# Kernel tuning notes

Measured on AMD Instinct MI355X. Metric: run time of the kernel, lower is better.

Reference implementation:

```python
import jax, jax.numpy as jnp
import numpy as np

DIM = 1024
NUM_HEAVY = 1024
N_ITERS = 50
EPS = 1.0
FETCH_K_RATIO = 9.0 / 8.0


def rms_norm(x, gamma):
    # F.normalize(x, dim=-1) * sqrt(d) * gamma
    norm = jnp.maximum(jnp.linalg.norm(x, axis=-1, keepdims=True), 1e-12)
    return (x / norm) * (x.shape[-1] ** 0.5) * gamma


def feed_forward(x, gamma, w1, b1, w2, b2):
    h = jax.nn.gelu(rms_norm(x, gamma) @ w1 + b1, approximate=False)
    return h @ w2 + b2


def coor_descent(s, k, n_iters, eps):
    # Wright et al. coordinate descent routing scores (eps_decay=1 -> constant eps)
    logk = jnp.log(jnp.asarray(k, dtype=s.dtype))

    def step(ab, _):
        a, b = ab
        sb = (s + b) / eps
        a = eps * (logk - jax.scipy.special.logsumexp(sb, axis=-1, keepdims=True))
        b = -jax.nn.relu(s + a)
        return (a, b), None

    a0 = jnp.zeros_like(s[..., :1])
    b0 = -s
    (a, b), _ = jax.lax.scan(step, (a0, b0), None, length=n_iters)
    return jnp.exp((s + a + b) / eps)


def setup_inputs() -> dict:
    key = jax.random.key(0)
    ks = jax.random.split(key, 8)
    b, n, d = 4, 8192, DIM
    dl, dh = int(d * 0.5), d * 4
    u = lambda k, shape, fan_in: jax.random.uniform(k, shape, jnp.float32, -1.0, 1.0) / np.sqrt(fan_in)
    return {
        "x": jax.random.normal(ks[0], (b, n, d), jnp.float32),
        "routing_token": jax.random.normal(ks[1], (d,), jnp.float32),
        "light_gamma": jnp.ones((d,), jnp.float32),
        "light_w1": u(ks[2], (d, dl), d),
        "light_b1": jnp.zeros((dl,), jnp.float32),
        "light_w2": u(ks[3], (dl, d), dl),
        "light_b2": jnp.zeros((d,), jnp.float32),
        "heavy_gamma": jnp.ones((d,), jnp.float32),
        "heavy_w1": u(ks[4], (d, dh), d),
        "heavy_b1": jnp.zeros((dh,), jnp.float32),
        "heavy_w2": u(ks[5], (dh, d), dh),
        "heavy_b2": jnp.zeros((d,), jnp.float32),
    }


def reference(x, routing_token, light_gamma, light_w1, light_b1, light_w2, light_b2,
              heavy_gamma, heavy_w1, heavy_b1, heavy_w2, heavy_b2):
    b, n, d = x.shape
    # light branch over all tokens
    light_out = feed_forward(x, light_gamma, light_w1, light_b1, light_w2, light_b2)

    # coordinate-descent router (single routing token)
    s = jnp.einsum('bnd,d->bn', x, routing_token)
    effective_k = min(NUM_HEAVY * FETCH_K_RATIO, n)
    scores = coor_descent(s, effective_k, N_ITERS, EPS)
    sel_scores, sel_idx = jax.lax.top_k(scores, NUM_HEAVY)  # [b, k]
    # straight-through: forward value 1.0, gradient flows through sel_scores
    sel_scores = sel_scores + jax.lax.stop_gradient(1.0 - sel_scores)

    # gather -> heavy FFN -> scale -> scatter back
    routed = jnp.take_along_axis(x, sel_idx[..., None], axis=1)  # [b, k, d]
    routed_out = feed_forward(routed, heavy_gamma, heavy_w1, heavy_b1, heavy_w2, heavy_b2)
    routed_out = routed_out * sel_scores[..., None]
    batch_idx = jnp.arange(b)[:, None]
    heavy_out = jnp.zeros_like(x).at[batch_idx, sel_idx].set(routed_out)

    return light_out + heavy_out
```

## Files before the change

kernel.cpp:

```cpp
#include <hip/hip_runtime.h>
#include <hip/hip_bf16.h>
#include <math.h>

#define DIMD   1024
#define NBATCH 4
#define NSEQ   8192
#define NTOK   (NBATCH * NSEQ)
#define NHEAVY 1024
#define NSEL   (NBATCH * NHEAVY)
#define DLIGHT 512
#define DHEAVY 4096
#define NITERS 50
#define BK     64

typedef __attribute__((ext_vector_type(8))) short short8;
typedef __attribute__((ext_vector_type(4))) float f32x4;
typedef __attribute__((ext_vector_type(4))) unsigned short u16x4;

__device__ __forceinline__ unsigned short f2bf(float f) {
    __hip_bfloat16 h = __float2bfloat16(f);
    union { __hip_bfloat16 h; unsigned short u; } cvt;
    cvt.h = h;
    return cvt.u;
}

__device__ __forceinline__ float bf2f(unsigned short u) {
    return __uint_as_float((unsigned)u << 16);
}

__device__ __forceinline__ float gelu_fast(float x) {
    float ax = fabsf(x) * 0.7071067811865475f;
    float t = 1.0f / fmaf(0.3275911f, ax, 1.0f);
    float p = fmaf(t, 1.061405429f, -1.453152027f);
    p = fmaf(t, p, 1.421413741f);
    p = fmaf(t, p, -0.284496736f);
    p = fmaf(t, p, 0.254829592f);
    p = p * t;
    float e = __expf(-ax * ax);
    float erf_abs = fmaf(-p, e, 1.0f);
    float erf = copysignf(erf_abs, x);
    return 0.5f * x * (1.0f + erf);
}

__device__ __forceinline__ void gload_lds16(const void* g, void* l) {
    __builtin_amdgcn_global_load_lds(
        (const __attribute__((address_space(1))) void*)g,
        (__attribute__((address_space(3))) void*)l,
        16, 0, 0);
}

__global__ __launch_bounds__(256) void fused_init(
    const float* __restrict__ lw1, const float* __restrict__ lw2,
    const float* __restrict__ hw1, const float* __restrict__ hw2,
    const float* __restrict__ lgamma, const float* __restrict__ hgamma,
    short* __restrict__ wl1t, short* __restrict__ wl2t,
    short* __restrict__ wh1t, short* __restrict__ wh2t,
    const float* __restrict__ x, const float* __restrict__ rt,
    unsigned short* __restrict__ xb, float* __restrict__ sc,
    double* __restrict__ s_out, int* __restrict__ inv) {
    __shared__ float tile[32][33];
    __shared__ float red[4];
    __shared__ double redd[4];
    int b = blockIdx.x;
    int tid = threadIdx.x;

    const float* cin = nullptr; short* cout = nullptr; const float* cg = nullptr;
    int cK = 0, cN = 0, cnx = 0, cb = 0;
    if (b < 512)        { cin = lw1; cout = wl1t; cg = lgamma; cK = DIMD;   cN = DLIGHT; cnx = 16;  cb = b; }
    else if (b < 1024)  { cin = lw2; cout = wl2t; cg = nullptr; cK = DLIGHT; cN = DIMD;  cnx = 32;  cb = b - 512; }
    else if (b < 5120)  { cin = hw1; cout = wh1t; cg = hgamma; cK = DIMD;   cN = DHEAVY; cnx = 128; cb = b - 1024; }
    else if (b < 9216)  { cin = hw2; cout = wh2t; cg = nullptr; cK = DHEAVY; cN = DIMD;  cnx = 32;  cb = b - 5120; }

    if (cin) {
        int n0 = (cb % cnx) * 32, k0 = (cb / cnx) * 32;
        int tx = tid & 31, ty = tid >> 5;
        #pragma unroll
        for (int j = 0; j < 4; j++) {
            int k = k0 + ty + 8 * j;
            float g = cg ? cg[k] : 1.0f;
            tile[ty + 8 * j][tx] = cin[(size_t)k * cN + (n0 + tx)] * g;
        }
        __syncthreads();
        #pragma unroll
        for (int j = 0; j < 4; j++)
            cout[(size_t)(n0 + ty + 8 * j) * cK + (k0 + tx)] =
                (short)f2bf(tile[tx][ty + 8 * j]);
        return;
    }

    int t = b - 9216;
    const float4* xr = (const float4*)(x + (size_t)t * DIMD);
    float4 v = xr[tid];
    ushort4 pk;
    pk.x = f2bf(v.x); pk.y = f2bf(v.y); pk.z = f2bf(v.z); pk.w = f2bf(v.w);
    ((ushort4*)(xb + (size_t)t * DIMD))[tid] = pk;

    float ss = v.x * v.x + v.y * v.y + v.z * v.z + v.w * v.w;
    float4 rv = ((const float4*)rt)[tid];
    double sd = (double)v.x * rv.x + (double)v.y * rv.y + (double)v.z * rv.z + (double)v.w * rv.w;
    #pragma unroll
    for (int off = 32; off > 0; off >>= 1) {
        ss += __shfl_down(ss, off);
        sd += __shfl_down(sd, off);
    }
    if ((tid & 63) == 0) { red[tid >> 6] = ss; redd[tid >> 6] = sd; }
    __syncthreads();
    if (tid == 0) {
        s_out[t] = redd[0] + redd[1] + redd[2] + redd[3];
        float tot = red[0] + red[1] + red[2] + red[3];
        sc[t] = 32.0f / fmaxf(sqrtf(tot), 1e-12f);
        inv[t] = -1;
    }
}

__global__ __launch_bounds__(256) void mega_kern(
    const double* __restrict__ s, int* __restrict__ sel, int* __restrict__ inv,
    const short* __restrict__ A, const short* __restrict__ Bt,
    const float* __restrict__ bias, const float* __restrict__ sc,
    __hip_bfloat16* __restrict__ outb) {
    __shared__ alignas(16) char smem[65536 + 64];
    short (*As)[128 * 64] = reinterpret_cast<short (*)[128 * 64]>(smem);
    short (*Bs)[128 * 64] = reinterpret_cast<short (*)[128 * 64]>(smem + 32768);
    int tid = threadIdx.x;

    if (blockIdx.x < 4) {
        int r = blockIdx.x;
        int lw = tid & 63, w = tid >> 6;
        double* redd = (double*)(smem + 65536);
        const double* sr = s + (size_t)r * NSEQ;
        double es[32];
        #pragma unroll
        for (int i = 0; i < 32; i++) es[i] = exp(sr[tid + i * 256]);
        const double Kk = 1152.0;
        double ea = exp(log(Kk) - log((double)NSEQ));
        for (int it = 1; it < NITERS; it++) {
            double loc = 0.0;
            #pragma unroll
            for (int i = 0; i < 32; i++) {
                double p = es[i] * ea;
                loc += (p < 1.0 ? p : 1.0);
            }
            #pragma unroll
            for (int off = 32; off > 0; off >>= 1) loc += __shfl_down(loc, off);
            int pb = (it & 1) * 4;
            if (lw == 0) redd[pb + w] = loc;
            __syncthreads();
            double S = redd[pb] + redd[pb + 1] + redd[pb + 2] + redd[pb + 3];
            ea = ea * (Kk / S);
        }
        double a = log(ea);
        __syncthreads();
        if (tid >= 64) return;

        int l = tid;
        double* sw = (double*)smem;
        int cnt = 0;
        for (int base = 0; base < NSEQ; base += 64) {
            int idx = base + l;
            double v = sr[idx];
            bool sat = (v + a) >= 0.0;
            sw[idx] = sat ? -1.0e300 : v;
            unsigned long long m = __ballot(sat);
            int pre = __popcll(m & ((1ull << l) - 1ull));
            if (sat) {
                int slot = cnt + pre;
                if (slot < NHEAVY) {
                    sel[r * NHEAVY + slot] = r * NSEQ + idx;
                    inv[r * NSEQ + idx] = r * NHEAVY + slot;
                }
            }
            cnt += (int)__popcll(m);
        }
        for (int slot = cnt; slot < NHEAVY; slot++) {
            double best = -1.0e301; int bidx = NSEQ;
            for (int i = 0; i < NSEQ / 64; i++) {
                int idx = i * 64 + l;
                double v = sw[idx];
                if (v > best) { best = v; bidx = idx; }
            }
            #pragma unroll
            for (int off = 32; off > 0; off >>= 1) {
                double ov = __shfl_down(best, off);
                int oi = __shfl_down(bidx, off);
                if (ov > best || (ov == best && oi < bidx)) { best = ov; bidx = oi; }
            }
            bidx = __shfl(bidx, 0);
            if (l == 0) {
                sel[r * NHEAVY + slot] = r * NSEQ + bidx;
                inv[r * NSEQ + bidx] = r * NHEAVY + slot;
                sw[bidx] = -1.0e300;
            }
        }
        return;
    }

    const int N = DLIGHT, K = DIMD;
    int gid = blockIdx.x - 4;
    int id = (gid & 7) * (1024 >> 3) + (gid >> 3);
    int nx = N / 128;
    int bxi = id % nx, byi = id / nx;
    int l = tid & 63, w = tid >> 6;
    int wr = w >> 1, wc = w & 1;
    int bn0 = bxi * 128, bm0 = byi * 128;

    f32x4 zero = {0.f, 0.f, 0.f, 0.f};
    f32x4 acc[4][4];
    #pragma unroll
    for (int i = 0; i < 4; i++)
        #pragma unroll
        for (int j = 0; j < 4; j++) acc[i][j] = zero;

    const short* AgC[4];
    const short* BgC[4];
    #pragma unroll
    for (int c = 0; c < 4; c++) {
        int p = c * 4096 + tid * 16;
        int o = p ^ (((p >> 7) & 7) << 4);
        int lrow = o >> 7, colb = o & 127;
        AgC[c] = A + (size_t)(bm0 + lrow) * K + (colb >> 1);
        BgC[c] = Bt + (size_t)(bn0 + lrow) * K + (colb >> 1);
    }
    const int sbase = (tid & ~63) * 8;

    auto stage = [&](int b, int k0) {
        #pragma unroll
        for (int c = 0; c < 4; c++) {
            gload_lds16(AgC[c] + k0, &As[b][sbase + c * 2048]);
            gload_lds16(BgC[c] + k0, &Bs[b][sbase + c * 2048]);
        }
    };

    const int lr16 = l & 15;
    const int swzm = (lr16 & 7) << 4;
    const int colkm[2] = { ((l >> 4) * 16) ^ swzm, (((l >> 4) * 16) + 64) ^ swzm };

    int nt = K / 64;
    stage(0, 0);
    for (int t = 0; t < nt; ++t) {
        int cur = t & 1;
        if (t + 1 < nt) {
            stage(cur ^ 1, (t + 1) * 64);
            asm volatile("s_waitcnt vmcnt(8)" ::: "memory");
        } else {
            asm volatile("s_waitcnt vmcnt(0)" ::: "memory");
        }
        __builtin_amdgcn_s_barrier();
        asm volatile("" ::: "memory");
        const char* aBuf = (const char*)&As[cur][0];
        const char* bBuf = (const char*)&Bs[cur][0];
        #pragma unroll
        for (int kk = 0; kk < 2; kk++) {
            short8 af[4], bf[4];
            #pragma unroll
            for (int i = 0; i < 4; i++) {
                af[i] = *reinterpret_cast<const short8*>(aBuf + (wr * 64 + i * 16 + lr16) * 128 + colkm[kk]);
                bf[i] = *reinterpret_cast<const short8*>(bBuf + (wc * 64 + i * 16 + lr16) * 128 + colkm[kk]);
            }
            #pragma unroll
            for (int mi = 0; mi < 4; mi++)
                #pragma unroll
                for (int ni = 0; ni < 4; ni++)
                    acc[mi][ni] = __builtin_amdgcn_mfma_f32_16x16x32_bf16(bf[ni], af[mi], acc[mi][ni], 0, 0, 0);
        }
        if (t + 1 < nt) {
            asm volatile("" ::: "memory");
            __builtin_amdgcn_s_barrier();
            asm volatile("" ::: "memory");
        }
    }

    int orow0 = bm0 + wr * 64, ocol0 = bn0 + wc * 64;
    const int lq = (l >> 4) * 4;
    #pragma unroll
    for (int mi = 0; mi < 4; mi++) {
        int row = orow0 + mi * 16 + lr16;
        float scv = sc[row];
        #pragma unroll
        for (int ni = 0; ni < 4; ni++) {
            int c0 = ocol0 + ni * 16 + lq;
            f32x4 bv = *reinterpret_cast<const f32x4*>(bias + c0);
            u16x4 pk;
            #pragma unroll
            for (int rg = 0; rg < 4; rg++)
                pk[rg] = f2bf(gelu_fast(fmaf(scv, acc[mi][ni][rg], bv[rg])));
            *reinterpret_cast<u16x4*>((unsigned short*)outb + (size_t)row * N + c0) = pk;
        }
    }
}

__global__ __launch_bounds__(256) void reduce_hv_kern(
    const unsigned short* __restrict__ phb, const float* __restrict__ hb2,
    float* __restrict__ hv, int nsk) {
    int h = blockIdx.x;
    int c0 = threadIdx.x * 4;
    f32x4 acc = *reinterpret_cast<const f32x4*>(hb2 + c0);
    for (int j = 0; j < nsk; j++) {
        u16x4 p = *reinterpret_cast<const u16x4*>(phb + ((size_t)j * NSEL + h) * DIMD + c0);
        #pragma unroll
        for (int rg = 0; rg < 4; rg++) acc[rg] += bf2f(p[rg]);
    }
    *reinterpret_cast<f32x4*>(hv + (size_t)h * DIMD + c0) = acc;
}

template <int EPI, bool GATHER>
__global__ __launch_bounds__(512) void gemm256(
    const short* __restrict__ A, const short* __restrict__ Bt,
    const float* __restrict__ bias,
    const float* __restrict__ sc, const int* __restrict__ sel,
    const int* __restrict__ inv, const float* __restrict__ hv,
    float* __restrict__ outf, __hip_bfloat16* __restrict__ outb,
    int M, int N, int K) {
    __shared__ alignas(16) short As[2][2][128 * 64];
    __shared__ alignas(16) short Bs[2][2][128 * 64];

    int nx = gridDim.x, ny = gridDim.y;
    int nwg = nx * ny * gridDim.z;
    int id = ((int)blockIdx.z * ny + blockIdx.y) * nx + blockIdx.x;
    if ((nwg & 7) == 0) id = (id & 7) * (nwg >> 3) + (id >> 3);
    int bxi = id % nx; int rem = id / nx;
    int byi = rem % ny; int bz = rem / ny;
    int klen = K / (int)gridDim.z, k0base = bz * klen;
    int bn0 = bxi * 256, bm0 = byi * 256;

    int tid = threadIdx.x;
    int l = tid & 63, w = tid >> 6;
    int wr = w >> 2, wc = w & 3;

    f32x4 zero = {0.f, 0.f, 0.f, 0.f};
    f32x4 acc[8][4];
    #pragma unroll
    for (int i = 0; i < 8; i++)
        #pragma unroll
        for (int j = 0; j < 4; j++) acc[i][j] = zero;

    const short* aSrc[2][2];
    const short* bSrc[2][2];
    #pragma unroll
    for (int h = 0; h < 2; h++)
        #pragma unroll
        for (int j = 0; j < 2; j++) {
            int p = j * 8192 + tid * 16;
            int o = p ^ (((p >> 7) & 7) << 4);
            int lrow = o >> 7, colb = o & 127;
            int agrow = bm0 + h * 128 + lrow;
            int garow = GATHER ? sel[agrow] : agrow;
            aSrc[h][j] = A + (size_t)garow * K + (colb >> 1);
            bSrc[h][j] = Bt + (size_t)(bn0 + h * 128 + lrow) * K + (colb >> 1);
        }

    auto stageA = [&](int b, int h, int kof) {
        #pragma unroll
        for (int j = 0; j < 2; j++)
            gload_lds16(aSrc[h][j] + kof, &As[b][h][j * 4096 + w * 512]);
    };
    auto stageB = [&](int b, int h, int kof) {
        #pragma unroll
        for (int j = 0; j < 2; j++)
            gload_lds16(bSrc[h][j] + kof, &Bs[b][h][j * 4096 + w * 512]);
    };

    int nt = klen / BK;
    stageA(0, 0, k0base); stageA(0, 1, k0base);
    stageB(0, 0, k0base); stageB(0, 1, k0base);
    if (nt > 1) {
        stageB(1, 0, k0base + BK); stageB(1, 1, k0base + BK);
        asm volatile("s_waitcnt vmcnt(4)" ::: "memory");
    } else {
        asm volatile("s_waitcnt vmcnt(0)" ::: "memory");
    }
    __builtin_amdgcn_s_barrier();

    const int lr = l & 15;
    const int swz = (lr & 7) << 4;
    const int rbase = lr * 128;
    const int colk[2] = { (((l >> 4) * 16)) ^ swz, (((l >> 4) * 16) + 64) ^ swz };

    short8 bfr[4][2];
    for (int t = 0; t < nt; ++t) {
        int d = t & 1;
        const char* aHalf = (const char*)(&As[d][wr][0]);
        const char* bHalf = (const char*)(&Bs[d][wc >> 1][0]) + (wc & 1) * 8192;
        #pragma unroll
        for (int ph = 0; ph < 2; ph++) {
            if (ph == 0) {
                #pragma unroll
                for (int ni = 0; ni < 4; ni++)
                    #pragma unroll
                    for (int kk = 0; kk < 2; kk++)
                        bfr[ni][kk] = *reinterpret_cast<const short8*>(bHalf + rbase + ni * 2048 + colk[kk]);
            }
            short8 afr[4][2];
            #pragma unroll
            for (int m2 = 0; m2 < 4; m2++)
                #pragma unroll
                for (int kk = 0; kk < 2; kk++)
                    afr[m2][kk] = *reinterpret_cast<const short8*>(aHalf + rbase + (ph * 4 + m2) * 2048 + colk[kk]);
            if (ph == 0) {
                if (t + 1 < nt) {
                    stageA(d ^ 1, 0, k0base + (t + 1) * BK);
                    stageA(d ^ 1, 1, k0base + (t + 1) * BK);
                }
            } else {
                if (t + 2 < nt) {
                    stageB(d, 0, k0base + (t + 2) * BK);
                    stageB(d, 1, k0base + (t + 2) * BK);
                    asm volatile("s_waitcnt vmcnt(4)" ::: "memory");
                } else {
                    asm volatile("s_waitcnt vmcnt(0)" ::: "memory");
                }
            }
            __builtin_amdgcn_s_barrier();
            asm volatile("s_waitcnt lgkmcnt(0)" ::: "memory");
            __builtin_amdgcn_s_setprio(1);
            #pragma unroll
            for (int m2 = 0; m2 < 4; m2++)
                #pragma unroll
                for (int ni = 0; ni < 4; ni++)
                    #pragma unroll
                    for (int kk = 0; kk < 2; kk++)
                        acc[ph * 4 + m2][ni] = __builtin_amdgcn_mfma_f32_16x16x32_bf16(
                            bfr[ni][kk], afr[m2][kk], acc[ph * 4 + m2][ni], 0, 0, 0);
            __builtin_amdgcn_s_setprio(0);
            __builtin_amdgcn_s_barrier();
        }
    }

    int orow0 = bm0 + wr * 128, ocol0 = bn0 + wc * 64;
    const int lq = (l >> 4) * 4;
    #pragma unroll
    for (int mi = 0; mi < 8; mi++) {
        int row = orow0 + mi * 16 + lr;
        float scv = 0.0f;
        int iv = -1;
        if (EPI == 0) scv = sc[GATHER ? sel[row] : row];
        if (EPI == 3) iv = inv[row];
        #pragma unroll
        for (int ni = 0; ni < 4; ni++) {
            int c0 = ocol0 + ni * 16 + lq;
            if (EPI == 0) {
                f32x4 bv = *reinterpret_cast<const f32x4*>(bias + c0);
                u16x4 pk;
                #pragma unroll
                for (int rg = 0; rg < 4; rg++)
                    pk[rg] = f2bf(gelu_fast(fmaf(scv, acc[mi][ni][rg], bv[rg])));
                *reinterpret_cast<u16x4*>((unsigned short*)outb + (size_t)row * N + c0) = pk;
            } else if (EPI == 2) {
                u16x4 pk;
                #pragma unroll
                for (int rg = 0; rg < 4; rg++) pk[rg] = f2bf(acc[mi][ni][rg]);
                *reinterpret_cast<u16x4*>((unsigned short*)outb + ((size_t)bz * M + row) * (size_t)N + c0) = pk;
            } else {
                f32x4 bv = *reinterpret_cast<const f32x4*>(bias + c0);
                f32x4 v = acc[mi][ni] + bv;
                if (iv >= 0) {
                    f32x4 hvv = *reinterpret_cast<const f32x4*>(hv + (size_t)iv * DIMD + c0);
                    v = v + hvv;
                }
                __builtin_nontemporal_store(v, reinterpret_cast<f32x4*>(outf + (size_t)row * N + c0));
            }
        }
    }
}

extern "C" void kernel_launch(void* const* d_in, const int* in_sizes, int n_in,
                              void* d_out, int out_size, void* d_ws, size_t ws_size,
                              hipStream_t stream) {
    (void)in_sizes; (void)n_in; (void)out_size;
    const float* x      = (const float*)d_in[0];
    const float* rt     = (const float*)d_in[1];
    const float* lgamma = (const float*)d_in[2];
    const float* lw1    = (const float*)d_in[3];
    const float* lb1    = (const float*)d_in[4];
    const float* lw2    = (const float*)d_in[5];
    const float* lb2    = (const float*)d_in[6];
    const float* hgamma = (const float*)d_in[7];
    const float* hw1    = (const float*)d_in[8];
    const float* hb1    = (const float*)d_in[9];
    const float* hw2    = (const float*)d_in[10];
    const float* hb2    = (const float*)d_in[11];
    float* out = (float*)d_out;

    auto rnd = [](size_t b) { return (b + 255) & ~(size_t)255; };
    size_t fixed = rnd(NTOK * sizeof(double))
                 + rnd(NSEL * sizeof(int))
                 + rnd(NTOK * sizeof(int))
                 + rnd(NTOK * sizeof(float))
                 + rnd((size_t)DLIGHT * DIMD * 2)
                 + rnd((size_t)DIMD * DLIGHT * 2)
                 + rnd((size_t)DHEAVY * DIMD * 2)
                 + rnd((size_t)DIMD * DHEAVY * 2)
                 + rnd((size_t)NTOK * DIMD * 2)
                 + rnd((size_t)NSEL * DHEAVY * 2)
                 + rnd((size_t)NTOK * DLIGHT * 2)
                 + rnd((size_t)NSEL * DIMD * 4);
    int nsk = 4;
    while (nsk > 1 && fixed + rnd((size_t)nsk * NSEL * DIMD * 2) > ws_size) nsk >>= 1;

    char* base = (char*)d_ws;
    size_t off = 0;
    auto alloc = [&](size_t bytes) -> void* {
        void* p = base + off;
        off += rnd(bytes);
        return p;
    };
    double* s     = (double*)alloc(NTOK * sizeof(double));
    int*    sel   = (int*)alloc(NSEL * sizeof(int));
    int*    inv   = (int*)alloc(NTOK * sizeof(int));
    float*  sc    = (float*)alloc(NTOK * sizeof(float));
    short*  wl1t  = (short*)alloc((size_t)DLIGHT * DIMD * 2);
    short*  wl2t  = (short*)alloc((size_t)DIMD * DLIGHT * 2);
    short*  wh1t  = (short*)alloc((size_t)DHEAVY * DIMD * 2);
    short*  wh2t  = (short*)alloc((size_t)DIMD * DHEAVY * 2);
    short*  xb    = (short*)alloc((size_t)NTOK * DIMD * 2);
    short*  hh    = (short*)alloc((size_t)NSEL * DHEAVY * 2);
    short*  hl    = (short*)alloc((size_t)NTOK * DLIGHT * 2);
    float*  hv    = (float*)alloc((size_t)NSEL * DIMD * 4);
    short*  phb   = (short*)alloc((size_t)nsk * NSEL * DIMD * 2);

    fused_init<<<9216 + NTOK, 256, 0, stream>>>(
        lw1, lw2, hw1, hw2, lgamma, hgamma,
        wl1t, wl2t, wh1t, wh2t,
        x, rt, (unsigned short*)xb, sc, s, inv);

    mega_kern<<<4 + 1024, 256, 0, stream>>>(
        s, sel, inv, xb, wl1t, lb1, sc, (__hip_bfloat16*)hl);

    gemm256<0, true><<<dim3(DHEAVY / 256, NSEL / 256), 512, 0, stream>>>(
        xb, wh1t, hb1, sc, sel, nullptr, nullptr,
        nullptr, (__hip_bfloat16*)hh, NSEL, DHEAVY, DIMD);
    gemm256<2, false><<<dim3(DIMD / 256, NSEL / 256, nsk), 512, 0, stream>>>(
        hh, wh2t, nullptr, nullptr, nullptr, nullptr, nullptr,
        nullptr, (__hip_bfloat16*)phb, NSEL, DIMD, DHEAVY);
    reduce_hv_kern<<<NSEL, 256, 0, stream>>>((const unsigned short*)phb, hb2, hv, nsk);

    gemm256<3, false><<<dim3(DIMD / 256, NTOK / 256), 512, 0, stream>>>(
        hl, wl2t, lb2, nullptr, nullptr, inv, hv,
        out, nullptr, NTOK, DIMD, DLIGHT);
}
```

Measured before the change: 290.8 us.

## Simplify GEMM pipelines to single-barrier double buffering with full prefetch

Both GEMM kernels move to a plain double-buffered loop. Each iteration issues all global->LDS loads for the next tile up front, computes the current tile, then waits with vmcnt(0) and takes one barrier. This replaces the split A/B staging with partial vmcnt waits and two barriers per phase in the large GEMM. The mega kernel's reduction scratch now reuses the start of shared memory instead of an extra 64 bytes. Fewer barriers cut synchronisation overhead, but waiting for all loads at the end of each tile may expose load latency that the staggered scheme hid.

```diff
diff --git a/kernel.cpp b/kernel.cpp
--- a/kernel.cpp
+++ b/kernel.cpp
@@ -118,7 +118,7 @@
     const short* __restrict__ A, const short* __restrict__ Bt,
     const float* __restrict__ bias, const float* __restrict__ sc,
     __hip_bfloat16* __restrict__ outb) {
-    __shared__ alignas(16) char smem[65536 + 64];
+    __shared__ alignas(16) char smem[65536];
     short (*As)[128 * 64] = reinterpret_cast<short (*)[128 * 64]>(smem);
     short (*Bs)[128 * 64] = reinterpret_cast<short (*)[128 * 64]>(smem + 32768);
     int tid = threadIdx.x;
@@ -126,7 +126,7 @@
     if (blockIdx.x < 4) {
         int r = blockIdx.x;
         int lw = tid & 63, w = tid >> 6;
-        double* redd = (double*)(smem + 65536);
+        double* redd = (double*)smem;
         const double* sr = s + (size_t)r * NSEQ;
         double es[32];
         #pragma unroll
@@ -236,18 +236,14 @@
 
     int nt = K / 64;
     stage(0, 0);
+    asm volatile("s_waitcnt vmcnt(0)" ::: "memory");
+    __builtin_amdgcn_s_barrier();
     for (int t = 0; t < nt; ++t) {
         int cur = t & 1;
-        if (t + 1 < nt) {
-            stage(cur ^ 1, (t + 1) * 64);
-            asm volatile("s_waitcnt vmcnt(8)" ::: "memory");
-        } else {
-            asm volatile("s_waitcnt vmcnt(0)" ::: "memory");
-        }
-        __builtin_amdgcn_s_barrier();
-        asm volatile("" ::: "memory");
+        if (t + 1 < nt) stage(cur ^ 1, (t + 1) * 64);
         const char* aBuf = (const char*)&As[cur][0];
         const char* bBuf = (const char*)&Bs[cur][0];
+        __builtin_amdgcn_s_setprio(1);
         #pragma unroll
         for (int kk = 0; kk < 2; kk++) {
             short8 af[4], bf[4];
@@ -262,10 +258,10 @@
                 for (int ni = 0; ni < 4; ni++)
                     acc[mi][ni] = __builtin_amdgcn_mfma_f32_16x16x32_bf16(bf[ni], af[mi], acc[mi][ni], 0, 0, 0);
         }
+        __builtin_amdgcn_s_setprio(0);
         if (t + 1 < nt) {
-            asm volatile("" ::: "memory");
+            asm volatile("s_waitcnt vmcnt(0)" ::: "memory");
             __builtin_amdgcn_s_barrier();
-            asm volatile("" ::: "memory");
         }
     }
 
@@ -348,26 +344,20 @@
             bSrc[h][j] = Bt + (size_t)(bn0 + h * 128 + lrow) * K + (colb >> 1);
         }
 
-    auto stageA = [&](int b, int h, int kof) {
-        #pragma unroll
-        for (int j = 0; j < 2; j++)
-            gload_lds16(aSrc[h][j] + kof, &As[b][h][j * 4096 + w * 512]);
+    auto stageAll = [&](int b, int kof) {
+        #pragma unroll
+        for (int j = 0; j < 2; j++) gload_lds16(aSrc[0][j] + kof, &As[b][0][j * 4096 + w * 512]);
+        #pragma unroll
+        for (int j = 0; j < 2; j++) gload_lds16(aSrc[1][j] + kof, &As[b][1][j * 4096 + w * 512]);
+        #pragma unroll
+        for (int j = 0; j < 2; j++) gload_lds16(bSrc[0][j] + kof, &Bs[b][0][j * 4096 + w * 512]);
+        #pragma unroll
+        for (int j = 0; j < 2; j++) gload_lds16(bSrc[1][j] + kof, &Bs[b][1][j * 4096 + w * 512]);
     };
-    auto stageB = [&](int b, int h, int kof) {
-        #pragma unroll
-        for (int j = 0; j < 2; j++)
-            gload_lds16(bSrc[h][j] + kof, &Bs[b][h][j * 4096 + w * 512]);
-    };
 
     int nt = klen / BK;
-    stageA(0, 0, k0base); stageA(0, 1, k0base);
-    stageB(0, 0, k0base); stageB(0, 1, k0base);
-    if (nt > 1) {
-        stageB(1, 0, k0base + BK); stageB(1, 1, k0base + BK);
-        asm volatile("s_waitcnt vmcnt(4)" ::: "memory");
-    } else {
-        asm volatile("s_waitcnt vmcnt(0)" ::: "memory");
-    }
+    stageAll(0, k0base);
+    asm volatile("s_waitcnt vmcnt(0)" ::: "memory");
     __builtin_amdgcn_s_barrier();
 
     const int lr = l & 15;
@@ -375,42 +365,25 @@
     const int rbase = lr * 128;
     const int colk[2] = { (((l >> 4) * 16)) ^ swz, (((l >> 4) * 16) + 64) ^ swz };
 
-    short8 bfr[4][2];
     for (int t = 0; t < nt; ++t) {
         int d = t & 1;
+        if (t + 1 < nt) stageAll(d ^ 1, k0base + (t + 1) * BK);
         const char* aHalf = (const char*)(&As[d][wr][0]);
         const char* bHalf = (const char*)(&Bs[d][wc >> 1][0]) + (wc & 1) * 8192;
+        short8 bfr[4][2];
+        #pragma unroll
+        for (int ni = 0; ni < 4; ni++)
+            #pragma unroll
+            for (int kk = 0; kk < 2; kk++)
+                bfr[ni][kk] = *reinterpret_cast<const short8*>(bHalf + rbase + ni * 2048 + colk[kk]);
         #pragma unroll
         for (int ph = 0; ph < 2; ph++) {
-            if (ph == 0) {
-                #pragma unroll
-                for (int ni = 0; ni < 4; ni++)
-                    #pragma unroll
-                    for (int kk = 0; kk < 2; kk++)
-                        bfr[ni][kk] = *reinterpret_cast<const short8*>(bHalf + rbase + ni * 2048 + colk[kk]);
-            }
             short8 afr[4][2];
             #pragma unroll
             for (int m2 = 0; m2 < 4; m2++)
                 #pragma unroll
                 for (int kk = 0; kk < 2; kk++)
                     afr[m2][kk] = *reinterpret_cast<const short8*>(aHalf + rbase + (ph * 4 + m2) * 2048 + colk[kk]);
-            if (ph == 0) {
-                if (t + 1 < nt) {
-                    stageA(d ^ 1, 0, k0base + (t + 1) * BK);
-                    stageA(d ^ 1, 1, k0base + (t + 1) * BK);
-                }
-            } else {
-                if (t + 2 < nt) {
-                    stageB(d, 0, k0base + (t + 2) * BK);
-                    stageB(d, 1, k0base + (t + 2) * BK);
-                    asm volatile("s_waitcnt vmcnt(4)" ::: "memory");
-                } else {
-                    asm volatile("s_waitcnt vmcnt(0)" ::: "memory");
-                }
-            }
-            __builtin_amdgcn_s_barrier();
-            asm volatile("s_waitcnt lgkmcnt(0)" ::: "memory");
             __builtin_amdgcn_s_setprio(1);
             #pragma unroll
             for (int m2 = 0; m2 < 4; m2++)
@@ -421,6 +394,9 @@
                         acc[ph * 4 + m2][ni] = __builtin_amdgcn_mfma_f32_16x16x32_bf16(
                             bfr[ni][kk], afr[m2][kk], acc[ph * 4 + m2][ni], 0, 0, 0);
             __builtin_amdgcn_s_setprio(0);
+        }
+        if (t + 1 < nt) {
+            asm volatile("s_waitcnt vmcnt(0)" ::: "memory");
             __builtin_amdgcn_s_barrier();
         }
     }
```

New measurement: 311.8 us. 1.07x slower.
